# Optimization experiments

Measured on AMD Instinct MI355X. Metric: run time of the kernel, lower is better.

## Reference

```python
import math
import jax, jax.numpy as jnp
import numpy as np

N, D, E, H = 4096, 512, 64, 8
LN_EPS = 1e-5


def setup_inputs() -> dict:
    key = jax.random.key(0)
    ks = jax.random.split(key, 6)
    return {
        "x": jax.random.normal(ks[0], (N, D), jnp.float32),
        "wq": jax.random.normal(ks[1], (H, D, E), jnp.float32) * 0.05,
        "wk": jax.random.normal(ks[2], (H, D, E), jnp.float32) * 0.05,
        "wv": jax.random.normal(ks[3], (H, D, E), jnp.float32) * 0.05,
        "w_mh": jax.random.normal(ks[4], (H * E, D), jnp.float32) * 0.05,
        "ln1_g": jnp.ones((D,), jnp.float32),
        "ln1_b": jnp.zeros((D,), jnp.float32),
        "ffn_w": jax.random.normal(ks[5], (D, D), jnp.float32) * 0.05,  # torch Linear weight [out,in]
        "ffn_b": jnp.zeros((D,), jnp.float32),
        "ln2_g": jnp.ones((D,), jnp.float32),
        "ln2_b": jnp.zeros((D,), jnp.float32),
    }


def _layernorm(y, g, b):
    m = y.mean(-1, keepdims=True)
    v = ((y - m) ** 2).mean(-1, keepdims=True)
    return (y - m) * jax.lax.rsqrt(v + LN_EPS) * g + b


def reference(x, wq, wk, wv, w_mh, ln1_g, ln1_b, ffn_w, ffn_b, ln2_g, ln2_b):
    dk = math.sqrt(wk.shape[-1])  # sqrt(embedding_size), as in the torch code
    q = jnp.einsum('nd,hde->hne', x, wq)  # [H,N,E]
    k = jnp.einsum('nd,hde->hne', x, wk)
    v = jnp.einsum('nd,hde->hne', x, wv)
    scores = jax.nn.softmax(jnp.einsum('hne,hme->hnm', q, k) / dk, axis=-1)  # [H,N,N]
    z = jnp.einsum('hnm,hme->hne', scores, v)  # [H,N,E]
    concat_z = jnp.transpose(z, (1, 0, 2)).reshape(x.shape[0], -1)  # [N, H*E]
    transformed_z = concat_z @ w_mh  # [N, D]
    normed_z = _layernorm(transformed_z + x, ln1_g, ln1_b)
    out = normed_z @ ffn_w.T + ffn_b  # nn.Linear
    return _layernorm(out + normed_z, ln2_g, ln2_b)
```

## Files before the change

### kernel.cpp

```cpp
#include <hip/hip_runtime.h>

#define NN 4096
#define DD 512
#define EE 64
#define HH 8

typedef _Float16 f16;
typedef f16 f16x2 __attribute__((ext_vector_type(2)));
typedef f16 f16x4 __attribute__((ext_vector_type(4)));
typedef f16 f16x8 __attribute__((ext_vector_type(8)));
typedef float f32x4 __attribute__((ext_vector_type(4)));
typedef __fp16 fp16x2 __attribute__((ext_vector_type(2)));

__device__ __forceinline__ float hexp2(float x) { return __builtin_amdgcn_exp2f(x); }
__device__ __forceinline__ f16x2 pkrtz(float a, float b) {
    fp16x2 r = __builtin_amdgcn_cvt_pkrtz(a, b);
    return __builtin_bit_cast(f16x2, r);
}
union f16x4u { f16x4 v4; f16x2 v2[2]; };
union f16x8u { f16x8 v8; f16x2 v2[4]; };

__device__ void tile_transpose_cvt(const float* __restrict__ src, f16* __restrict__ dst,
                                   int R, int C, int bx, int by, int tid)
{
    __shared__ float t[32][33];
    const int tx = tid & 31, ty = tid >> 5;
    #pragma unroll
    for (int i = 0; i < 4; ++i) {
        int r = ty + i * 8;
        t[r][tx] = src[(size_t)(by + r) * C + bx + tx];
    }
    __syncthreads();
    #pragma unroll
    for (int i = 0; i < 4; ++i) {
        int c = ty + i * 8;
        dst[(size_t)(bx + c) * R + by + tx] = (f16)t[tx][c];
    }
}

__global__ __launch_bounds__(256) void prep_kernel(
    const float* __restrict__ x, const float* __restrict__ ffn_w,
    const float* __restrict__ wq, const float* __restrict__ wk, const float* __restrict__ wv,
    const float* __restrict__ w_mh,
    f16* __restrict__ xh, f16* __restrict__ ffnT, f16* __restrict__ wqkvT, f16* __restrict__ wmhT)
{
    const int job = blockIdx.y;
    const int tid = threadIdx.x;
    if (job == 0) {
        size_t i = ((size_t)blockIdx.x * 256 + tid) * 4;
        const size_t step = (size_t)256 * 256 * 4;
        for (; i < (size_t)NN * DD; i += step) {
            float4 t = *(const float4*)(x + i);
            f16x4 h = { (f16)t.x, (f16)t.y, (f16)t.z, (f16)t.w };
            *(f16x4*)(xh + i) = h;
        }
    } else if (job == 1) {
        size_t i = ((size_t)blockIdx.x * 256 + tid) * 4;
        float4 t = *(const float4*)(ffn_w + i);
        f16x4 h = { (f16)t.x, (f16)t.y, (f16)t.z, (f16)t.w };
        *(f16x4*)(ffnT + i) = h;
    } else if (job <= 4) {
        const float* src = (job == 2) ? wq : (job == 3) ? wk : wv;
        f16* dst = wqkvT + (size_t)(job - 2) * HH * EE * DD;
        const int z = blockIdx.x >> 5;
        const int tile = blockIdx.x & 31;
        tile_transpose_cvt(src + (size_t)z * DD * EE, dst + (size_t)z * DD * EE,
                           DD, EE, (tile & 1) * 32, (tile >> 1) * 32, tid);
    } else {
        const int tile = blockIdx.x;
        tile_transpose_cvt(w_mh, wmhT, DD, DD, (tile & 15) * 32, (tile >> 4) * 32, tid);
    }
}

__global__ __launch_bounds__(256) void qkv_mfma_kernel(
    const f16* __restrict__ A, const f16* __restrict__ BT,
    f16* __restrict__ qh, f16* __restrict__ kh, f16* __restrict__ vTh)
{
    __shared__ f16 As[2][64][72];
    __shared__ f16 Bs[2][64][72];
    const int tid = threadIdx.x;
    const int n0 = blockIdx.x * 64;
    const int cb = blockIdx.y;
    const int sel = cb >> 3, h = cb & 7;
    const f16* Arow = A + (size_t)n0 * DD;
    const f16* Brow = BT + (size_t)cb * 64 * DD;

    const int lane = tid & 63, wave = tid >> 6;
    const int l16 = lane & 15, quad = lane >> 4;
    const int m0 = wave * 16;

    const int r1 = tid >> 3, c1 = (tid & 7) * 8;
    const int r2 = (tid + 256) >> 3, c2 = ((tid + 256) & 7) * 8;

    f32x4 acc[4];
    #pragma unroll
    for (int t = 0; t < 4; ++t) acc[t] = (f32x4){0.f, 0.f, 0.f, 0.f};

    f16x8 a1 = *(const f16x8*)(Arow + (size_t)r1 * DD + c1);
    f16x8 a2 = *(const f16x8*)(Arow + (size_t)r2 * DD + c2);
    f16x8 b1 = *(const f16x8*)(Brow + (size_t)r1 * DD + c1);
    f16x8 b2 = *(const f16x8*)(Brow + (size_t)r2 * DD + c2);

    int buf = 0;
    for (int kt = 0; kt < DD; kt += 64) {
        *(f16x8*)(&As[buf][r1][c1]) = a1;
        *(f16x8*)(&As[buf][r2][c2]) = a2;
        *(f16x8*)(&Bs[buf][r1][c1]) = b1;
        *(f16x8*)(&Bs[buf][r2][c2]) = b2;
        __syncthreads();
        if (kt + 64 < DD) {
            a1 = *(const f16x8*)(Arow + (size_t)r1 * DD + kt + 64 + c1);
            a2 = *(const f16x8*)(Arow + (size_t)r2 * DD + kt + 64 + c2);
            b1 = *(const f16x8*)(Brow + (size_t)r1 * DD + kt + 64 + c1);
            b2 = *(const f16x8*)(Brow + (size_t)r2 * DD + kt + 64 + c2);
        }
        #pragma unroll
        for (int kk = 0; kk < 64; kk += 32) {
            f16x8 a = *(const f16x8*)(&As[buf][m0 + l16][kk + quad * 8]);
            #pragma unroll
            for (int t = 0; t < 4; ++t) {
                f16x8 b = *(const f16x8*)(&Bs[buf][t * 16 + l16][kk + quad * 8]);
                acc[t] = __builtin_amdgcn_mfma_f32_16x16x32_f16(a, b, acc[t], 0, 0, 0);
            }
        }
        buf ^= 1;
    }

    if (sel == 2) {
        #pragma unroll
        for (int t = 0; t < 4; ++t) {
            int e = t * 16 + l16;
            f16x4 v = { (f16)acc[t][0], (f16)acc[t][1], (f16)acc[t][2], (f16)acc[t][3] };
            *(f16x4*)(vTh + ((size_t)h * EE + e) * NN + n0 + m0 + quad * 4) = v;
        }
    } else {
        f16* o = (sel == 0) ? qh : kh;
        const float s = (sel == 0) ? 0.125f * 1.44269504088896f : 1.0f;
        #pragma unroll
        for (int r = 0; r < 4; ++r) {
            int row = n0 + m0 + quad * 4 + r;
            #pragma unroll
            for (int t = 0; t < 4; ++t)
                o[(size_t)h * NN * EE + (size_t)row * EE + t * 16 + l16] = (f16)(acc[t][r] * s);
        }
    }
}

#define BQ 128
#define BK 64
#define LK (BK + 12)

__global__ __launch_bounds__(256) void attn_mfma_kernel(
    const f16* __restrict__ q, const f16* __restrict__ k,
    const f16* __restrict__ vT, f16* __restrict__ Opart, float* __restrict__ lpart)
{
    __shared__ f16 Ks[BK][LK];
    __shared__ f16 VsT[EE][LK];

    const int tid = threadIdx.x;
    const int h = blockIdx.y;
    const int n0 = blockIdx.x * BQ;
    const int sp = blockIdx.z;
    const int nsp = gridDim.z;
    const int wave = tid >> 6;
    const int lane = tid & 63;
    const int l16 = lane & 15;
    const int quad = lane >> 4;
    const int m0 = wave * 16;

    const f16* qh = q + (size_t)h * NN * EE;
    const f16* kh = k + (size_t)h * NN * EE;
    const f16* vh = vT + (size_t)h * NN * EE;

    f16x8 qf[2][2];
    #pragma unroll
    for (int s = 0; s < 2; ++s) {
        const f16* qb = qh + (size_t)(n0 + s * 64 + m0 + l16) * EE;
        qf[s][0] = *(const f16x8*)(qb + quad * 8);
        qf[s][1] = *(const f16x8*)(qb + 32 + quad * 8);
    }

    float lp[2] = {0.f, 0.f};
    f32x4 O[2][4];
    #pragma unroll
    for (int s = 0; s < 2; ++s)
        #pragma unroll
        for (int t = 0; t < 4; ++t) O[s][t] = (f32x4){0.f, 0.f, 0.f, 0.f};

    const int span = NN / nsp;
    const int k_begin = sp * span;
    const int k_end = k_begin + span;

    const int srow = tid >> 3, sc8 = (tid & 7) * 8;
    const int srow2 = (tid + 256) >> 3, sc82 = ((tid + 256) & 7) * 8;
    #define KPERM(kk_) (((kk_) & 0x23) | (((kk_) & 0x04) << 2) | (((kk_) & 0x18) >> 1))
    const int prow1 = KPERM(srow), prow2 = KPERM(srow2);

    f16x8 kr0 = *(const f16x8*)(kh + (size_t)(k_begin + srow) * EE + sc8);
    f16x8 kr1 = *(const f16x8*)(kh + (size_t)(k_begin + srow2) * EE + sc82);
    f16x8 vr0 = *(const f16x8*)(vh + (size_t)srow * NN + k_begin + sc8);
    f16x8 vr1 = *(const f16x8*)(vh + (size_t)srow2 * NN + k_begin + sc82);

    for (int kt = k_begin; kt < k_end; kt += BK) {
        __syncthreads();
        *(f16x8*)(&Ks[prow1][sc8]) = kr0;
        *(f16x8*)(&Ks[prow2][sc82]) = kr1;
        *(f16x8*)(&VsT[srow][sc8]) = vr0;
        *(f16x8*)(&VsT[srow2][sc82]) = vr1;
        __syncthreads();

        if (kt + BK < k_end) {
            kr0 = *(const f16x8*)(kh + (size_t)(kt + BK + srow) * EE + sc8);
            kr1 = *(const f16x8*)(kh + (size_t)(kt + BK + srow2) * EE + sc82);
            vr0 = *(const f16x8*)(vh + (size_t)srow * NN + kt + BK + sc8);
            vr1 = *(const f16x8*)(vh + (size_t)srow2 * NN + kt + BK + sc82);
        }

        f16x8 bf[2][2];
        #pragma unroll
        for (int t = 0; t < 4; ++t) {
            f16x8 a0 = *(const f16x8*)(&Ks[t * 16 + l16][quad * 8]);
            f16x8 a1 = *(const f16x8*)(&Ks[t * 16 + l16][32 + quad * 8]);
            #pragma unroll
            for (int s = 0; s < 2; ++s) {
                f32x4 st = {0.f, 0.f, 0.f, 0.f};
                st = __builtin_amdgcn_mfma_f32_16x16x32_f16(a0, qf[s][0], st, 0, 0, 0);
                st = __builtin_amdgcn_mfma_f32_16x16x32_f16(a1, qf[s][1], st, 0, 0, 0);
                float p0 = hexp2(st[0]);
                float p1 = hexp2(st[1]);
                float p2 = hexp2(st[2]);
                float p3 = hexp2(st[3]);
                lp[s] += (p0 + p1) + (p2 + p3);
                f16x2* bp = (f16x2*)&bf[s][t >> 1];
                const int o2 = (t & 1) * 2;
                bp[o2 + 0] = pkrtz(p0, p1);
                bp[o2 + 1] = pkrtz(p2, p3);
            }
        }

        #pragma unroll
        for (int te = 0; te < 4; ++te) {
            f16x8 v0 = *(const f16x8*)(&VsT[te * 16 + l16][quad * 8]);
            f16x8 v1 = *(const f16x8*)(&VsT[te * 16 + l16][32 + quad * 8]);
            #pragma unroll
            for (int s = 0; s < 2; ++s) {
                O[s][te] = __builtin_amdgcn_mfma_f32_16x16x32_f16(v0, bf[s][0], O[s][te], 0, 0, 0);
                O[s][te] = __builtin_amdgcn_mfma_f32_16x16x32_f16(v1, bf[s][1], O[s][te], 0, 0, 0);
            }
        }
    }

    #pragma unroll
    for (int s = 0; s < 2; ++s) {
        float l = lp[s];
        l += __shfl_xor(l, 16);
        l += __shfl_xor(l, 32);
        const int row = n0 + s * 64 + m0 + l16;
        if (quad == 0)
            lpart[(size_t)sp * HH * NN + (size_t)h * NN + row] = l;
        const float inv = 1.f / l;
        f16* obase = Opart + ((size_t)sp * NN + row) * DD + h * EE;
        #pragma unroll
        for (int te = 0; te < 4; ++te) {
            f16x4u v;
            v.v2[0] = pkrtz(O[s][te][0] * inv, O[s][te][1] * inv);
            v.v2[1] = pkrtz(O[s][te][2] * inv, O[s][te][3] * inv);
            *(f16x4*)(obase + te * 16 + quad * 4) = v.v4;
        }
    }
}

template<int NSP>
__global__ __launch_bounds__(256) void gemmz_mfma_kernel(
    const f16* __restrict__ Opart, const float* __restrict__ lpart,
    const f16* __restrict__ BT, const f16* __restrict__ resid16, f16* __restrict__ out)
{
    __shared__ f16 As[2][64][72];
    __shared__ f16 Bs[2][64][72];
    const int tid = threadIdx.x;
    const int n0 = blockIdx.x * 64;
    const int j0 = blockIdx.y * 64;
    const f16* Brow = BT + (size_t)j0 * DD;

    const int lane = tid & 63, wave = tid >> 6;
    const int l16 = lane & 15, quad = lane >> 4;
    const int m0 = wave * 16;

    const int r1 = tid >> 3, c1 = (tid & 7) * 8;
    const int r2 = (tid + 256) >> 3, c2 = ((tid + 256) & 7) * 8;

    f32x4 acc[4];
    #pragma unroll
    for (int t = 0; t < 4; ++t) acc[t] = (f32x4){0.f, 0.f, 0.f, 0.f};

    f16x8 op1[NSP], op2[NSP];
    #pragma unroll
    for (int s = 0; s < NSP; ++s) {
        op1[s] = *(const f16x8*)(Opart + ((size_t)s * NN + n0 + r1) * DD + c1);
        op2[s] = *(const f16x8*)(Opart + ((size_t)s * NN + n0 + r2) * DD + c2);
    }
    f16x8 b1 = *(const f16x8*)(Brow + (size_t)r1 * DD + c1);
    f16x8 b2 = *(const f16x8*)(Brow + (size_t)r2 * DD + c2);

    int buf = 0;
    for (int kt = 0; kt < DD; kt += 64) {
        const int h = kt >> 6;
        float lw1[NSP], lw2[NSP], s1 = 0.f, s2 = 0.f;
        #pragma unroll
        for (int s = 0; s < NSP; ++s) {
            lw1[s] = lpart[(size_t)s * HH * NN + (size_t)h * NN + n0 + r1];
            lw2[s] = lpart[(size_t)s * HH * NN + (size_t)h * NN + n0 + r2];
            s1 += lw1[s]; s2 += lw2[s];
        }
        const float i1 = 1.f / s1, i2 = 1.f / s2;
        float aw1[8], aw2[8];
        #pragma unroll
        for (int i = 0; i < 8; ++i) { aw1[i] = 0.f; aw2[i] = 0.f; }
        #pragma unroll
        for (int s = 0; s < NSP; ++s) {
            const float w1 = lw1[s] * i1, w2 = lw2[s] * i2;
            #pragma unroll
            for (int i = 0; i < 8; ++i) {
                aw1[i] += w1 * (float)op1[s][i];
                aw2[i] += w2 * (float)op2[s][i];
            }
        }
        f16x8u av1, av2;
        #pragma unroll
        for (int i = 0; i < 4; ++i) {
            av1.v2[i] = pkrtz(aw1[2 * i], aw1[2 * i + 1]);
            av2.v2[i] = pkrtz(aw2[2 * i], aw2[2 * i + 1]);
        }
        *(f16x8*)(&As[buf][r1][c1]) = av1.v8;
        *(f16x8*)(&As[buf][r2][c2]) = av2.v8;
        *(f16x8*)(&Bs[buf][r1][c1]) = b1;
        *(f16x8*)(&Bs[buf][r2][c2]) = b2;
        __syncthreads();
        if (kt + 64 < DD) {
            #pragma unroll
            for (int s = 0; s < NSP; ++s) {
                op1[s] = *(const f16x8*)(Opart + ((size_t)s * NN + n0 + r1) * DD + kt + 64 + c1);
                op2[s] = *(const f16x8*)(Opart + ((size_t)s * NN + n0 + r2) * DD + kt + 64 + c2);
            }
            b1 = *(const f16x8*)(Brow + (size_t)r1 * DD + kt + 64 + c1);
            b2 = *(const f16x8*)(Brow + (size_t)r2 * DD + kt + 64 + c2);
        }
        #pragma unroll
        for (int kk = 0; kk < 64; kk += 32) {
            f16x8 a = *(const f16x8*)(&As[buf][m0 + l16][kk + quad * 8]);
            #pragma unroll
            for (int t = 0; t < 4; ++t) {
                f16x8 b = *(const f16x8*)(&Bs[buf][t * 16 + l16][kk + quad * 8]);
                acc[t] = __builtin_amdgcn_mfma_f32_16x16x32_f16(a, b, acc[t], 0, 0, 0);
            }
        }
        buf ^= 1;
    }

    #pragma unroll
    for (int r = 0; r < 4; ++r) {
        int row = n0 + m0 + quad * 4 + r;
        #pragma unroll
        for (int t = 0; t < 4; ++t) {
            int col = j0 + t * 16 + l16;
            float v = acc[t][r] + (float)resid16[(size_t)row * DD + col];
            out[(size_t)row * DD + col] = (f16)v;
        }
    }
}

__global__ __launch_bounds__(256) void gemm_mfma_kernel(
    const f16* __restrict__ A, const f16* __restrict__ BT,
    const float* __restrict__ bias, const f16* __restrict__ resid16,
    f16* __restrict__ out)
{
    __shared__ f16 As[2][64][72];
    __shared__ f16 Bs[2][64][72];
    const int tid = threadIdx.x;
    const int n0 = blockIdx.x * 64;
    const int j0 = blockIdx.y * 64;
    const f16* Arow = A + (size_t)n0 * DD;
    const f16* Brow = BT + (size_t)j0 * DD;

    const int lane = tid & 63, wave = tid >> 6;
    const int l16 = lane & 15, quad = lane >> 4;
    const int m0 = wave * 16;

    const int r1 = tid >> 3, c1 = (tid & 7) * 8;
    const int r2 = (tid + 256) >> 3, c2 = ((tid + 256) & 7) * 8;

    f32x4 acc[4];
    #pragma unroll
    for (int t = 0; t < 4; ++t) acc[t] = (f32x4){0.f, 0.f, 0.f, 0.f};

    f16x8 a1 = *(const f16x8*)(Arow + (size_t)r1 * DD + c1);
    f16x8 a2 = *(const f16x8*)(Arow + (size_t)r2 * DD + c2);
    f16x8 b1 = *(const f16x8*)(Brow + (size_t)r1 * DD + c1);
    f16x8 b2 = *(const f16x8*)(Brow + (size_t)r2 * DD + c2);

    int buf = 0;
    for (int kt = 0; kt < DD; kt += 64) {
        *(f16x8*)(&As[buf][r1][c1]) = a1;
        *(f16x8*)(&As[buf][r2][c2]) = a2;
        *(f16x8*)(&Bs[buf][r1][c1]) = b1;
        *(f16x8*)(&Bs[buf][r2][c2]) = b2;
        __syncthreads();
        if (kt + 64 < DD) {
            a1 = *(const f16x8*)(Arow + (size_t)r1 * DD + kt + 64 + c1);
            a2 = *(const f16x8*)(Arow + (size_t)r2 * DD + kt + 64 + c2);
            b1 = *(const f16x8*)(Brow + (size_t)r1 * DD + kt + 64 + c1);
            b2 = *(const f16x8*)(Brow + (size_t)r2 * DD + kt + 64 + c2);
        }
        #pragma unroll
        for (int kk = 0; kk < 64; kk += 32) {
            f16x8 a = *(const f16x8*)(&As[buf][m0 + l16][kk + quad * 8]);
            #pragma unroll
            for (int t = 0; t < 4; ++t) {
                f16x8 b = *(const f16x8*)(&Bs[buf][t * 16 + l16][kk + quad * 8]);
                acc[t] = __builtin_amdgcn_mfma_f32_16x16x32_f16(a, b, acc[t], 0, 0, 0);
            }
        }
        buf ^= 1;
    }

    #pragma unroll
    for (int r = 0; r < 4; ++r) {
        int row = n0 + m0 + quad * 4 + r;
        #pragma unroll
        for (int t = 0; t < 4; ++t) {
            int col = j0 + t * 16 + l16;
            float v = acc[t][r];
            if (bias)    v += bias[col];
            if (resid16) v += (float)resid16[(size_t)row * DD + col];
            out[(size_t)row * DD + col] = (f16)v;
        }
    }
}

__global__ __launch_bounds__(256) void ln_kernel(
    const f16* __restrict__ y, const float* __restrict__ g, const float* __restrict__ b,
    f16* __restrict__ oh, float* __restrict__ of)
{
    const int lane = threadIdx.x & 63, wave = threadIdx.x >> 6;
    const int row = blockIdx.x * 4 + wave;
    f16x8 v = *(const f16x8*)(y + (size_t)row * DD + lane * 8);
    float vf[8];
    float s = 0.f, q = 0.f;
    #pragma unroll
    for (int i = 0; i < 8; ++i) {
        vf[i] = (float)v[i];
        s += vf[i];
        q += vf[i] * vf[i];
    }
    #pragma unroll
    for (int o = 1; o < 64; o <<= 1) { s += __shfl_xor(s, o); q += __shfl_xor(q, o); }
    float mean = s * (1.f / DD);
    float var = q * (1.f / DD) - mean * mean;
    float inv = rsqrtf(var + 1e-5f);

    f32x4 g0 = *(const f32x4*)(g + lane * 8);
    f32x4 g1 = *(const f32x4*)(g + lane * 8 + 4);
    f32x4 b0 = *(const f32x4*)(b + lane * 8);
    f32x4 b1 = *(const f32x4*)(b + lane * 8 + 4);
    float o8[8];
    #pragma unroll
    for (int i = 0; i < 4; ++i) {
        o8[i]     = (vf[i] - mean) * inv * g0[i] + b0[i];
        o8[i + 4] = (vf[i + 4] - mean) * inv * g1[i] + b1[i];
    }
    if (oh) {
        f16x8 hv;
        #pragma unroll
        for (int i = 0; i < 8; ++i) hv[i] = (f16)o8[i];
        *(f16x8*)(oh + (size_t)row * DD + lane * 8) = hv;
    }
    if (of) {
        f32x4 f0 = { o8[0], o8[1], o8[2], o8[3] };
        f32x4 f1 = { o8[4], o8[5], o8[6], o8[7] };
        *(f32x4*)(of + (size_t)row * DD + lane * 8) = f0;
        *(f32x4*)(of + (size_t)row * DD + lane * 8 + 4) = f1;
    }
}

extern "C" void kernel_launch(void* const* d_in, const int* in_sizes, int n_in,
                              void* d_out, int out_size, void* d_ws, size_t ws_size,
                              hipStream_t stream) {
    const float* x     = (const float*)d_in[0];
    const float* wq    = (const float*)d_in[1];
    const float* wk    = (const float*)d_in[2];
    const float* wv    = (const float*)d_in[3];
    const float* w_mh  = (const float*)d_in[4];
    const float* ln1_g = (const float*)d_in[5];
    const float* ln1_b = (const float*)d_in[6];
    const float* ffn_w = (const float*)d_in[7];
    const float* ffn_b = (const float*)d_in[8];
    const float* ln2_g = (const float*)d_in[9];
    const float* ln2_b = (const float*)d_in[10];
    float* out = (float*)d_out;

    const size_t poolBytes = ((size_t)3 * HH * EE * DD + 2 * (size_t)DD * DD
                            + 3 * (size_t)HH * NN * EE + 3 * (size_t)NN * DD) * 2;
    int SP = 2;
    {
        size_t need4 = (size_t)4 * NN * DD * 2 + (size_t)4 * HH * NN * 4 + poolBytes + 4096;
        if (ws_size >= need4) SP = 4;
    }

    char* base = (char*)d_ws;
    f16* Opart = (f16*)base;
    float* lpart = (float*)(base + (size_t)SP * NN * DD * 2);
    size_t regionA = (size_t)SP * NN * DD * 2 + (size_t)SP * HH * NN * 4;
    regionA = (regionA + 255) & ~(size_t)255;
    f16* p = (f16*)(base + regionA);
    f16* wqkvT  = p; p += (size_t)3 * HH * EE * DD;
    f16* wmhT   = p; p += (size_t)DD * DD;
    f16* ffnT   = p; p += (size_t)DD * DD;
    f16* qh     = p; p += (size_t)HH * NN * EE;
    f16* kh     = p; p += (size_t)HH * NN * EE;
    f16* vTh    = p; p += (size_t)HH * NN * EE;
    f16* y16    = p; p += (size_t)NN * DD;
    f16* nzh    = p; p += (size_t)NN * DD;
    f16* xh     = p; p += (size_t)NN * DD;

    prep_kernel<<<dim3(256, 6), 256, 0, stream>>>(x, ffn_w, wq, wk, wv, w_mh,
                                                  xh, ffnT, wqkvT, wmhT);

    qkv_mfma_kernel<<<dim3(NN / 64, 24), 256, 0, stream>>>(xh, wqkvT, qh, kh, vTh);
    attn_mfma_kernel<<<dim3(NN / BQ, HH, SP), 256, 0, stream>>>(qh, kh, vTh, Opart, lpart);
    if (SP == 4)
        gemmz_mfma_kernel<4><<<dim3(NN / 64, DD / 64), 256, 0, stream>>>(Opart, lpart, wmhT, xh, y16);
    else
        gemmz_mfma_kernel<2><<<dim3(NN / 64, DD / 64), 256, 0, stream>>>(Opart, lpart, wmhT, xh, y16);
    ln_kernel<<<dim3(NN / 4), 256, 0, stream>>>(y16, ln1_g, ln1_b, nzh, nullptr);
    gemm_mfma_kernel<<<dim3(NN / 64, DD / 64), 256, 0, stream>>>(nzh, ffnT, ffn_b, nzh, y16);
    ln_kernel<<<dim3(NN / 4), 256, 0, stream>>>(y16, ln2_g, ln2_b, nullptr, out);
}
```

Measured before the change: 181.8 us.

## Fuse LayerNorm1 into GEMM epilogue/prologue via partial row statistics

```diff
diff --git a/kernel.cpp b/kernel.cpp
--- a/kernel.cpp
+++ b/kernel.cpp
@@ -19,6 +19,7 @@
 }
 union f16x4u { f16x4 v4; f16x2 v2[2]; };
 union f16x8u { f16x8 v8; f16x2 v2[4]; };
+union f32x8u { float a[8]; f32x4 v[2]; };
 
 __device__ void tile_transpose_cvt(const float* __restrict__ src, f16* __restrict__ dst,
                                    int R, int C, int bx, int by, int tid)
@@ -158,8 +159,8 @@
     __shared__ f16 VsT[EE][LK];
 
     const int tid = threadIdx.x;
-    const int h = blockIdx.y;
-    const int n0 = blockIdx.x * BQ;
+    const int h = blockIdx.x;
+    const int n0 = blockIdx.y * BQ;
     const int sp = blockIdx.z;
     const int nsp = gridDim.z;
     const int wave = tid >> 6;
@@ -273,7 +274,126 @@
 template<int NSP>
 __global__ __launch_bounds__(256) void gemmz_mfma_kernel(
     const f16* __restrict__ Opart, const float* __restrict__ lpart,
-    const f16* __restrict__ BT, const f16* __restrict__ resid16, f16* __restrict__ out)
+    const f16* __restrict__ BT, const f16* __restrict__ resid16,
+    f16* __restrict__ out, float* __restrict__ pstat)
+{
+    __shared__ f16 As[2][64][72];
+    __shared__ f16 Bs[2][64][72];
+    const int tid = threadIdx.x;
+    const int n0 = blockIdx.x * 64;
+    const int jb = blockIdx.y;
+    const int j0 = jb * 64;
+    const f16* Brow = BT + (size_t)j0 * DD;
+
+    const int lane = tid & 63, wave = tid >> 6;
+    const int l16 = lane & 15, quad = lane >> 4;
+    const int m0 = wave * 16;
+
+    const int r1 = tid >> 3, c1 = (tid & 7) * 8;
+    const int r2 = (tid + 256) >> 3, c2 = ((tid + 256) & 7) * 8;
+
+    f32x4 acc[4];
+    #pragma unroll
+    for (int t = 0; t < 4; ++t) acc[t] = (f32x4){0.f, 0.f, 0.f, 0.f};
+
+    f16x8 op1[NSP], op2[NSP];
+    #pragma unroll
+    for (int s = 0; s < NSP; ++s) {
+        op1[s] = *(const f16x8*)(Opart + ((size_t)s * NN + n0 + r1) * DD + c1);
+        op2[s] = *(const f16x8*)(Opart + ((size_t)s * NN + n0 + r2) * DD + c2);
+    }
+    f16x8 b1 = *(const f16x8*)(Brow + (size_t)r1 * DD + c1);
+    f16x8 b2 = *(const f16x8*)(Brow + (size_t)r2 * DD + c2);
+
+    int buf = 0;
+    for (int kt = 0; kt < DD; kt += 64) {
+        const int h = kt >> 6;
+        float lw1[NSP], lw2[NSP], s1 = 0.f, s2 = 0.f;
+        #pragma unroll
+        for (int s = 0; s < NSP; ++s) {
+            lw1[s] = lpart[(size_t)s * HH * NN + (size_t)h * NN + n0 + r1];
+            lw2[s] = lpart[(size_t)s * HH * NN + (size_t)h * NN + n0 + r2];
+            s1 += lw1[s]; s2 += lw2[s];
+        }
+        const float i1 = 1.f / s1, i2 = 1.f / s2;
+        float aw1[8], aw2[8];
+        #pragma unroll
+        for (int i = 0; i < 8; ++i) { aw1[i] = 0.f; aw2[i] = 0.f; }
+        #pragma unroll
+        for (int s = 0; s < NSP; ++s) {
+            const float w1 = lw1[s] * i1, w2 = lw2[s] * i2;
+            #pragma unroll
+            for (int i = 0; i < 8; ++i) {
+                aw1[i] += w1 * (float)op1[s][i];
+                aw2[i] += w2 * (float)op2[s][i];
+            }
+        }
+        f16x8u av1, av2;
+        #pragma unroll
+        for (int i = 0; i < 4; ++i) {
+            av1.v2[i] = pkrtz(aw1[2 * i], aw1[2 * i + 1]);
+            av2.v2[i] = pkrtz(aw2[2 * i], aw2[2 * i + 1]);
+        }
+        *(f16x8*)(&As[buf][r1][c1]) = av1.v8;
+        *(f16x8*)(&As[buf][r2][c2]) = av2.v8;
+        *(f16x8*)(&Bs[buf][r1][c1]) = b1;
+        *(f16x8*)(&Bs[buf][r2][c2]) = b2;
+        __syncthreads();
+        if (kt + 64 < DD) {
+            #pragma unroll
+            for (int s = 0; s < NSP; ++s) {
+                op1[s] = *(const f16x8*)(Opart + ((size_t)s * NN + n0 + r1) * DD + kt + 64 + c1);
+                op2[s] = *(const f16x8*)(Opart + ((size_t)s * NN + n0 + r2) * DD + kt + 64 + c2);
+            }
+            b1 = *(const f16x8*)(Brow + (size_t)r1 * DD + kt + 64 + c1);
+            b2 = *(const f16x8*)(Brow + (size_t)r2 * DD + kt + 64 + c2);
+        }
+        #pragma unroll
+        for (int kk = 0; kk < 64; kk += 32) {
+            f16x8 a = *(const f16x8*)(&As[buf][m0 + l16][kk + quad * 8]);
+            #pragma unroll
+            for (int t = 0; t < 4; ++t) {
+                f16x8 b = *(const f16x8*)(&Bs[buf][t * 16 + l16][kk + quad * 8]);
+                acc[t] = __builtin_amdgcn_mfma_f32_16x16x32_f16(a, b, acc[t], 0, 0, 0);
+            }
+        }
+        buf ^= 1;
+    }
+
+    float vv[4][4];
+    #pragma unroll
+    for (int r = 0; r < 4; ++r) {
+        int row = n0 + m0 + quad * 4 + r;
+        #pragma unroll
+        for (int t = 0; t < 4; ++t) {
+            int col = j0 + t * 16 + l16;
+            float v = acc[t][r] + (float)resid16[(size_t)row * DD + col];
+            vv[r][t] = v;
+            out[(size_t)row * DD + col] = (f16)v;
+        }
+    }
+    #pragma unroll
+    for (int r = 0; r < 4; ++r) {
+        float s = (vv[r][0] + vv[r][1]) + (vv[r][2] + vv[r][3]);
+        float q = (vv[r][0] * vv[r][0] + vv[r][1] * vv[r][1])
+                + (vv[r][2] * vv[r][2] + vv[r][3] * vv[r][3]);
+        s += __shfl_xor(s, 1); q += __shfl_xor(q, 1);
+        s += __shfl_xor(s, 2); q += __shfl_xor(q, 2);
+        s += __shfl_xor(s, 4); q += __shfl_xor(q, 4);
+        s += __shfl_xor(s, 8); q += __shfl_xor(q, 8);
+        if (l16 == 0) {
+            int row = n0 + m0 + quad * 4 + r;
+            pstat[(size_t)jb * NN + row] = s;
+            pstat[(size_t)(8 + jb) * NN + row] = q;
+        }
+    }
+}
+
+__global__ __launch_bounds__(256) void gemmln2_kernel(
+    const f16* __restrict__ y16, const float* __restrict__ pstat,
+    const f16* __restrict__ BT, const float* __restrict__ bias,
+    const float* __restrict__ lng, const float* __restrict__ lnb,
+    f16* __restrict__ out)
 {
     __shared__ f16 As[2][64][72];
     __shared__ f16 Bs[2][64][72];
@@ -289,47 +409,43 @@
     const int r1 = tid >> 3, c1 = (tid & 7) * 8;
     const int r2 = (tid + 256) >> 3, c2 = ((tid + 256) & 7) * 8;
 
+    float s1 = 0.f, q1 = 0.f, s2 = 0.f, q2 = 0.f;
+    #pragma unroll
+    for (int jb = 0; jb < 8; ++jb) {
+        s1 += pstat[(size_t)jb * NN + n0 + r1];
+        q1 += pstat[(size_t)(8 + jb) * NN + n0 + r1];
+        s2 += pstat[(size_t)jb * NN + n0 + r2];
+        q2 += pstat[(size_t)(8 + jb) * NN + n0 + r2];
+    }
+    const float m1 = s1 * (1.f / DD), m2 = s2 * (1.f / DD);
+    const float iv1 = rsqrtf(q1 * (1.f / DD) - m1 * m1 + 1e-5f);
+    const float iv2 = rsqrtf(q2 * (1.f / DD) - m2 * m2 + 1e-5f);
+
     f32x4 acc[4];
     #pragma unroll
     for (int t = 0; t < 4; ++t) acc[t] = (f32x4){0.f, 0.f, 0.f, 0.f};
 
-    f16x8 op1[NSP], op2[NSP];
-    #pragma unroll
-    for (int s = 0; s < NSP; ++s) {
-        op1[s] = *(const f16x8*)(Opart + ((size_t)s * NN + n0 + r1) * DD + c1);
-        op2[s] = *(const f16x8*)(Opart + ((size_t)s * NN + n0 + r2) * DD + c2);
-    }
+    f16x8 a1 = *(const f16x8*)(y16 + (size_t)(n0 + r1) * DD + c1);
+    f16x8 a2 = *(const f16x8*)(y16 + (size_t)(n0 + r2) * DD + c2);
     f16x8 b1 = *(const f16x8*)(Brow + (size_t)r1 * DD + c1);
     f16x8 b2 = *(const f16x8*)(Brow + (size_t)r2 * DD + c2);
 
     int buf = 0;
     for (int kt = 0; kt < DD; kt += 64) {
-        const int h = kt >> 6;
-        float lw1[NSP], lw2[NSP], s1 = 0.f, s2 = 0.f;
-        #pragma unroll
-        for (int s = 0; s < NSP; ++s) {
-            lw1[s] = lpart[(size_t)s * HH * NN + (size_t)h * NN + n0 + r1];
-            lw2[s] = lpart[(size_t)s * HH * NN + (size_t)h * NN + n0 + r2];
-            s1 += lw1[s]; s2 += lw2[s];
-        }
-        const float i1 = 1.f / s1, i2 = 1.f / s2;
-        float aw1[8], aw2[8];
-        #pragma unroll
-        for (int i = 0; i < 8; ++i) { aw1[i] = 0.f; aw2[i] = 0.f; }
-        #pragma unroll
-        for (int s = 0; s < NSP; ++s) {
-            const float w1 = lw1[s] * i1, w2 = lw2[s] * i2;
-            #pragma unroll
-            for (int i = 0; i < 8; ++i) {
-                aw1[i] += w1 * (float)op1[s][i];
-                aw2[i] += w2 * (float)op2[s][i];
-            }
-        }
+        f32x8u gu, bu;
+        gu.v[0] = *(const f32x4*)(lng + kt + c1);
+        gu.v[1] = *(const f32x4*)(lng + kt + c1 + 4);
+        bu.v[0] = *(const f32x4*)(lnb + kt + c1);
+        bu.v[1] = *(const f32x4*)(lnb + kt + c1 + 4);
         f16x8u av1, av2;
         #pragma unroll
         for (int i = 0; i < 4; ++i) {
-            av1.v2[i] = pkrtz(aw1[2 * i], aw1[2 * i + 1]);
-            av2.v2[i] = pkrtz(aw2[2 * i], aw2[2 * i + 1]);
+            float x0 = ((float)a1[2 * i]     - m1) * iv1 * gu.a[2 * i]     + bu.a[2 * i];
+            float x1 = ((float)a1[2 * i + 1] - m1) * iv1 * gu.a[2 * i + 1] + bu.a[2 * i + 1];
+            float y0 = ((float)a2[2 * i]     - m2) * iv2 * gu.a[2 * i]     + bu.a[2 * i];
+            float y1 = ((float)a2[2 * i + 1] - m2) * iv2 * gu.a[2 * i + 1] + bu.a[2 * i + 1];
+            av1.v2[i] = pkrtz(x0, x1);
+            av2.v2[i] = pkrtz(y0, y1);
         }
         *(f16x8*)(&As[buf][r1][c1]) = av1.v8;
         *(f16x8*)(&As[buf][r2][c2]) = av2.v8;
@@ -337,11 +453,8 @@
         *(f16x8*)(&Bs[buf][r2][c2]) = b2;
         __syncthreads();
         if (kt + 64 < DD) {
-            #pragma unroll
-            for (int s = 0; s < NSP; ++s) {
-                op1[s] = *(const f16x8*)(Opart + ((size_t)s * NN + n0 + r1) * DD + kt + 64 + c1);
-                op2[s] = *(const f16x8*)(Opart + ((size_t)s * NN + n0 + r2) * DD + kt + 64 + c2);
-            }
+            a1 = *(const f16x8*)(y16 + (size_t)(n0 + r1) * DD + kt + 64 + c1);
+            a2 = *(const f16x8*)(y16 + (size_t)(n0 + r2) * DD + kt + 64 + c2);
             b1 = *(const f16x8*)(Brow + (size_t)r1 * DD + kt + 64 + c1);
             b2 = *(const f16x8*)(Brow + (size_t)r2 * DD + kt + 64 + c2);
         }
@@ -359,79 +472,20 @@
 
     #pragma unroll
     for (int r = 0; r < 4; ++r) {
-        int row = n0 + m0 + quad * 4 + r;
+        const int row = n0 + m0 + quad * 4 + r;
+        float ss = 0.f, qq = 0.f;
+        #pragma unroll
+        for (int jb = 0; jb < 8; ++jb) {
+            ss += pstat[(size_t)jb * NN + row];
+            qq += pstat[(size_t)(8 + jb) * NN + row];
+        }
+        const float mr = ss * (1.f / DD);
+        const float ir = rsqrtf(qq * (1.f / DD) - mr * mr + 1e-5f);
         #pragma unroll
         for (int t = 0; t < 4; ++t) {
-            int col = j0 + t * 16 + l16;
-            float v = acc[t][r] + (float)resid16[(size_t)row * DD + col];
-            out[(size_t)row * DD + col] = (f16)v;
-        }
-    }
-}
-
-__global__ __launch_bounds__(256) void gemm_mfma_kernel(
-    const f16* __restrict__ A, const f16* __restrict__ BT,
-    const float* __restrict__ bias, const f16* __restrict__ resid16,
-    f16* __restrict__ out)
-{
-    __shared__ f16 As[2][64][72];
-    __shared__ f16 Bs[2][64][72];
-    const int tid = threadIdx.x;
-    const int n0 = blockIdx.x * 64;
-    const int j0 = blockIdx.y * 64;
-    const f16* Arow = A + (size_t)n0 * DD;
-    const f16* Brow = BT + (size_t)j0 * DD;
-
-    const int lane = tid & 63, wave = tid >> 6;
-    const int l16 = lane & 15, quad = lane >> 4;
-    const int m0 = wave * 16;
-
-    const int r1 = tid >> 3, c1 = (tid & 7) * 8;
-    const int r2 = (tid + 256) >> 3, c2 = ((tid + 256) & 7) * 8;
-
-    f32x4 acc[4];
-    #pragma unroll
-    for (int t = 0; t < 4; ++t) acc[t] = (f32x4){0.f, 0.f, 0.f, 0.f};
-
-    f16x8 a1 = *(const f16x8*)(Arow + (size_t)r1 * DD + c1);
-    f16x8 a2 = *(const f16x8*)(Arow + (size_t)r2 * DD + c2);
-    f16x8 b1 = *(const f16x8*)(Brow + (size_t)r1 * DD + c1);
-    f16x8 b2 = *(const f16x8*)(Brow + (size_t)r2 * DD + c2);
-
-    int buf = 0;
-    for (int kt = 0; kt < DD; kt += 64) {
-        *(f16x8*)(&As[buf][r1][c1]) = a1;
-        *(f16x8*)(&As[buf][r2][c2]) = a2;
-        *(f16x8*)(&Bs[buf][r1][c1]) = b1;
-        *(f16x8*)(&Bs[buf][r2][c2]) = b2;
-        __syncthreads();
-        if (kt + 64 < DD) {
-            a1 = *(const f16x8*)(Arow + (size_t)r1 * DD + kt + 64 + c1);
-            a2 = *(const f16x8*)(Arow + (size_t)r2 * DD + kt + 64 + c2);
-            b1 = *(const f16x8*)(Brow + (size_t)r1 * DD + kt + 64 + c1);
-            b2 = *(const f16x8*)(Brow + (size_t)r2 * DD + kt + 64 + c2);
-        }
-        #pragma unroll
-        for (int kk = 0; kk < 64; kk += 32) {
-            f16x8 a = *(const f16x8*)(&As[buf][m0 + l16][kk + quad * 8]);
-            #pragma unroll
-            for (int t = 0; t < 4; ++t) {
-                f16x8 b = *(const f16x8*)(&Bs[buf][t * 16 + l16][kk + quad * 8]);
-                acc[t] = __builtin_amdgcn_mfma_f32_16x16x32_f16(a, b, acc[t], 0, 0, 0);
-            }
-        }
-        buf ^= 1;
-    }
-
-    #pragma unroll
-    for (int r = 0; r < 4; ++r) {
-        int row = n0 + m0 + quad * 4 + r;
-        #pragma unroll
-        for (int t = 0; t < 4; ++t) {
-            int col = j0 + t * 16 + l16;
-            float v = acc[t][r];
-            if (bias)    v += bias[col];
-            if (resid16) v += (float)resid16[(size_t)row * DD + col];
+            const int col = j0 + t * 16 + l16;
+            float nz = ((float)y16[(size_t)row * DD + col] - mr) * ir * lng[col] + lnb[col];
+            float v = acc[t][r] + bias[col] + nz;
             out[(size_t)row * DD + col] = (f16)v;
         }
     }
@@ -439,7 +493,7 @@
 
 __global__ __launch_bounds__(256) void ln_kernel(
     const f16* __restrict__ y, const float* __restrict__ g, const float* __restrict__ b,
-    f16* __restrict__ oh, float* __restrict__ of)
+    float* __restrict__ of)
 {
     const int lane = threadIdx.x & 63, wave = threadIdx.x >> 6;
     const int row = blockIdx.x * 4 + wave;
@@ -462,24 +516,14 @@
     f32x4 g1 = *(const f32x4*)(g + lane * 8 + 4);
     f32x4 b0 = *(const f32x4*)(b + lane * 8);
     f32x4 b1 = *(const f32x4*)(b + lane * 8 + 4);
-    float o8[8];
+    f32x4 f0, f1;
     #pragma unroll
     for (int i = 0; i < 4; ++i) {
-        o8[i]     = (vf[i] - mean) * inv * g0[i] + b0[i];
-        o8[i + 4] = (vf[i + 4] - mean) * inv * g1[i] + b1[i];
-    }
-    if (oh) {
-        f16x8 hv;
-        #pragma unroll
-        for (int i = 0; i < 8; ++i) hv[i] = (f16)o8[i];
-        *(f16x8*)(oh + (size_t)row * DD + lane * 8) = hv;
-    }
-    if (of) {
-        f32x4 f0 = { o8[0], o8[1], o8[2], o8[3] };
-        f32x4 f1 = { o8[4], o8[5], o8[6], o8[7] };
-        *(f32x4*)(of + (size_t)row * DD + lane * 8) = f0;
-        *(f32x4*)(of + (size_t)row * DD + lane * 8 + 4) = f1;
-    }
+        f0[i] = (vf[i] - mean) * inv * g0[i] + b0[i];
+        f1[i] = (vf[i + 4] - mean) * inv * g1[i] + b1[i];
+    }
+    *(f32x4*)(of + (size_t)row * DD + lane * 8) = f0;
+    *(f32x4*)(of + (size_t)row * DD + lane * 8 + 4) = f1;
 }
 
 extern "C" void kernel_launch(void* const* d_in, const int* in_sizes, int n_in,
@@ -499,7 +543,8 @@
     float* out = (float*)d_out;
 
     const size_t poolBytes = ((size_t)3 * HH * EE * DD + 2 * (size_t)DD * DD
-                            + 3 * (size_t)HH * NN * EE + 3 * (size_t)NN * DD) * 2;
+                            + 3 * (size_t)HH * NN * EE + 3 * (size_t)NN * DD) * 2
+                            + (size_t)16 * NN * 4;
     int SP = 2;
     {
         size_t need4 = (size_t)4 * NN * DD * 2 + (size_t)4 * HH * NN * 4 + poolBytes + 4096;
@@ -519,19 +564,19 @@
     f16* kh     = p; p += (size_t)HH * NN * EE;
     f16* vTh    = p; p += (size_t)HH * NN * EE;
     f16* y16    = p; p += (size_t)NN * DD;
-    f16* nzh    = p; p += (size_t)NN * DD;
+    f16* y2     = p; p += (size_t)NN * DD;
     f16* xh     = p; p += (size_t)NN * DD;
+    float* pstat = (float*)p;
 
     prep_kernel<<<dim3(256, 6), 256, 0, stream>>>(x, ffn_w, wq, wk, wv, w_mh,
                                                   xh, ffnT, wqkvT, wmhT);
 
     qkv_mfma_kernel<<<dim3(NN / 64, 24), 256, 0, stream>>>(xh, wqkvT, qh, kh, vTh);
-    attn_mfma_kernel<<<dim3(NN / BQ, HH, SP), 256, 0, stream>>>(qh, kh, vTh, Opart, lpart);
+    attn_mfma_kernel<<<dim3(HH, NN / BQ, SP), 256, 0, stream>>>(qh, kh, vTh, Opart, lpart);
     if (SP == 4)
-        gemmz_mfma_kernel<4><<<dim3(NN / 64, DD / 64), 256, 0, stream>>>(Opart, lpart, wmhT, xh, y16);
+        gemmz_mfma_kernel<4><<<dim3(NN / 64, DD / 64), 256, 0, stream>>>(Opart, lpart, wmhT, xh, y16, pstat);
     else
-        gemmz_mfma_kernel<2><<<dim3(NN / 64, DD / 64), 256, 0, stream>>>(Opart, lpart, wmhT, xh, y16);
-    ln_kernel<<<dim3(NN / 4), 256, 0, stream>>>(y16, ln1_g, ln1_b, nzh, nullptr);
-    gemm_mfma_kernel<<<dim3(NN / 64, DD / 64), 256, 0, stream>>>(nzh, ffnT, ffn_b, nzh, y16);
-    ln_kernel<<<dim3(NN / 4), 256, 0, stream>>>(y16, ln2_g, ln2_b, nullptr, out);
-}
+        gemmz_mfma_kernel<2><<<dim3(NN / 64, DD / 64), 256, 0, stream>>>(Opart, lpart, wmhT, xh, y16, pstat);
+    gemmln2_kernel<<<dim3(NN / 64, DD / 64), 256, 0, stream>>>(y16, pstat, ffnT, ffn_b, ln1_g, ln1_b, y2);
+    ln_kernel<<<dim3(NN / 4), 256, 0, stream>>>(y2, ln2_g, ln2_b, out);
+}
```

Measured after the change: 177.7 us. 2.3% less time.
